# Performance work log

Measured on AMD Instinct MI355X. Metric: run time of the kernel, lower is better.

## Reference

```python
import jax, jax.numpy as jnp
import numpy as np

DIM = 128
NUM_HEADS = 8
HEAD_DIM = DIM // NUM_HEADS
N_NODES = 50000
N_EDGES = 800000


def setup_inputs() -> dict:
    key = jax.random.key(0)
    ks = jax.random.split(key, 10)
    scale = 1.0 / np.sqrt(DIM)
    x = jax.random.normal(ks[0], (N_NODES, DIM), dtype=jnp.float32)
    edge_index = jax.random.randint(ks[1], (2, N_EDGES), 0, N_NODES, dtype=jnp.int64)
    Wq = jax.random.normal(ks[2], (DIM, DIM), dtype=jnp.float32) * scale
    bq = jnp.zeros((DIM,), dtype=jnp.float32)
    Wk = jax.random.normal(ks[3], (DIM, DIM), dtype=jnp.float32) * scale
    bk = jnp.zeros((DIM,), dtype=jnp.float32)
    Wv = jax.random.normal(ks[4], (DIM, DIM), dtype=jnp.float32) * scale
    bv = jnp.zeros((DIM,), dtype=jnp.float32)
    Wo = jax.random.normal(ks[5], (DIM, DIM), dtype=jnp.float32) * scale
    bo = jnp.zeros((DIM,), dtype=jnp.float32)
    return {"x": x, "edge_index": edge_index, "Wq": Wq, "bq": bq,
            "Wk": Wk, "bk": bk, "Wv": Wv, "bv": bv, "Wo": Wo, "bo": bo}


def reference(x, edge_index, Wq, bq, Wk, bk, Wv, bv, Wo, bo):
    n = x.shape[0]
    tgt = edge_index[0]  # softmax group / scatter destination
    src = edge_index[1]  # gather source
    # projections: torch nn.Linear -> x @ W.T + b
    q = (x @ Wq.T + bq).reshape(n, NUM_HEADS, HEAD_DIM)
    k = (x @ Wk.T + bk).reshape(n, NUM_HEADS, HEAD_DIM)
    v = (x @ Wv.T + bv).reshape(n, NUM_HEADS, HEAD_DIM)
    # edge-wise attention scores: [E, H]
    scores = jnp.einsum('ehd,ehd->eh', q[src], k[tgt]) / np.sqrt(HEAD_DIM).astype(np.float32)
    # segment softmax over edges grouped by target node
    m = jax.ops.segment_max(scores, tgt, num_segments=n)          # [N, H]
    m = jax.lax.stop_gradient(m)
    p = jnp.exp(scores - m[tgt])                                   # [E, H]
    s = jax.ops.segment_sum(p, tgt, num_segments=n)               # [N, H]
    probs = p / s[tgt]
    # weighted scatter-add of source values
    weighted = v[src] * probs[..., None]                           # [E, H, D]
    agg = jax.ops.segment_sum(weighted, tgt, num_segments=n)      # [N, H, D]
    out = agg.reshape(n, DIM) @ Wo.T + bo
    # dropout is identity in eval mode
    return out
```

## Files before the change

kernel.cpp:

```cpp
#include <hip/hip_runtime.h>
#include <hip/hip_bf16.h>
#include <math.h>

#define NN 50000
#define NE 800000
#define DIM 128
#define NH 8
#define HD 16
#define NTILE 3125
#define TPB 782
#define LROW 136
#define QVROW 256
#define SCAN_B 196

typedef short v8s __attribute__((ext_vector_type(8)));
typedef float v4f __attribute__((ext_vector_type(4)));

__device__ __forceinline__ unsigned pack2(float a, float b) {
    __hip_bfloat162 h = __float22bfloat162_rn(make_float2(a, b));
    return *reinterpret_cast<unsigned*>(&h);
}
__device__ __forceinline__ float blo(unsigned w) { return __uint_as_float(w << 16); }
__device__ __forceinline__ float bhi(unsigned w) { return __uint_as_float(w & 0xffff0000u); }

__device__ __forceinline__ void stage_w_lds(
    const float* __restrict__ Wg, unsigned short* __restrict__ Wl, int tid)
{
#pragma unroll
    for (int it = 0; it < 16; ++it) {
        int chunk = it * 256 + tid;
        int row = chunk >> 5, c4 = chunk & 31;
        float4 f = ((const float4*)Wg)[chunk];
        uint2 o = { pack2(f.x, f.y), pack2(f.z, f.w) };
        *(uint2*)(Wl + row * LROW + c4 * 4) = o;
    }
}

__global__ __launch_bounds__(256) void qkv_mfma_kernel(
    const float* __restrict__ x,
    const float* __restrict__ Wq, const float* __restrict__ Wk, const float* __restrict__ Wv,
    const float* __restrict__ bq, const float* __restrict__ bk, const float* __restrict__ bv,
    unsigned short* __restrict__ qvb, unsigned short* __restrict__ kb,
    const int* __restrict__ tgt, int* __restrict__ cnt)
{
    __shared__ unsigned short Wl[DIM * LROW];
    const int mat = blockIdx.x / TPB;
    const int tg  = blockIdx.x % TPB;
    const int tid = threadIdx.x;
    const int lane = tid & 63;
    const int warp = tid >> 6;
    const int m = lane & 15;
    const int quad = lane >> 4;

    const int gsize = 3 * TPB * 256;
    for (int e = blockIdx.x * 256 + tid; e < NE; e += gsize)
        atomicAdd(cnt + tgt[e], 1);

    const float* Wg = (mat == 0) ? Wq : (mat == 1) ? Wk : Wv;
    stage_w_lds(Wg, Wl, tid);
    __syncthreads();

    const int rt = tg * 4 + warp;
    if (rt >= NTILE) return;
    const int r0 = rt * 16;
    const int node = r0 + m;

    const float* bias_p = (mat == 0) ? bq : (mat == 1) ? bk : bv;

    v8s a[4];
#pragma unroll
    for (int kt = 0; kt < 4; ++kt) {
        const float4* xr = (const float4*)(x + (size_t)node * DIM + kt * 32 + quad * 8);
        float4 f0 = xr[0], f1 = xr[1];
        uint4 u = { pack2(f0.x, f0.y), pack2(f0.z, f0.w),
                    pack2(f1.x, f1.y), pack2(f1.z, f1.w) };
        a[kt] = *(v8s*)&u;
    }

#pragma unroll
    for (int nt = 0; nt < 8; ++nt) {
        v4f c = {0.f, 0.f, 0.f, 0.f};
#pragma unroll
        for (int kt = 0; kt < 4; ++kt) {
            v8s wf = *(const v8s*)(Wl + (nt * 16 + m) * LROW + kt * 32 + quad * 8);
            c = __builtin_amdgcn_mfma_f32_16x16x32_bf16(wf, a[kt], c, 0, 0, 0);
        }
        const int cbase = nt * 16 + quad * 4;
        float4 b4 = *(const float4*)(bias_p + cbase);
        float o0 = c[0] + b4.x, o1 = c[1] + b4.y;
        float o2 = c[2] + b4.z, o3 = c[3] + b4.w;
        if (mat == 1) {
            uint2 pk = { pack2(o0, o1), pack2(o2, o3) };
            *(uint2*)(kb + (size_t)node * DIM + cbase) = pk;
        } else {
            int p0 = 2 * cbase + ((mat == 2) ? 2 : 0);
            *(unsigned*)(qvb + (size_t)node * QVROW + p0)     = pack2(o0, o1);
            *(unsigned*)(qvb + (size_t)node * QVROW + p0 + 4) = pack2(o2, o3);
        }
    }
}

__global__ __launch_bounds__(256) void scan1_kernel(
    const int* __restrict__ cnt, int* __restrict__ off, int* __restrict__ bsum)
{
    __shared__ int ws4[4];
    const int tid = threadIdx.x, lane = tid & 63, wid = tid >> 6;
    int i = blockIdx.x * 256 + tid;
    int v0 = (i < NN) ? cnt[i] : 0;
    int incl = v0;
#pragma unroll
    for (int d = 1; d < 64; d <<= 1) {
        int t = __shfl_up(incl, d);
        if (lane >= d) incl += t;
    }
    if (lane == 63) ws4[wid] = incl;
    __syncthreads();
    int wexcl = 0;
#pragma unroll
    for (int t = 0; t < 3; ++t) if (t < wid) wexcl += ws4[t];
    if (i < NN) off[i] = wexcl + incl - v0;
    if (tid == 255) bsum[blockIdx.x] = wexcl + incl;
}

__global__ __launch_bounds__(256) void scan23_kernel(
    const int* __restrict__ bsum, int* __restrict__ off, int* __restrict__ cursor)
{
    __shared__ int ws4[4];
    __shared__ int base_s, total_s;
    const int tid = threadIdx.x, lane = tid & 63, wid = tid >> 6;
    int v0 = (tid < SCAN_B) ? bsum[tid] : 0;
    int incl = v0;
#pragma unroll
    for (int d = 1; d < 64; d <<= 1) {
        int t = __shfl_up(incl, d);
        if (lane >= d) incl += t;
    }
    if (lane == 63) ws4[wid] = incl;
    __syncthreads();
    int wexcl = 0;
#pragma unroll
    for (int t = 0; t < 3; ++t) if (t < wid) wexcl += ws4[t];
    int excl = wexcl + incl - v0;
    if (tid == blockIdx.x) base_s = excl;
    if (tid == SCAN_B - 1) total_s = excl + v0;
    __syncthreads();
    int i = blockIdx.x * 256 + tid;
    if (i < NN) {
        int t = off[i] + base_s;
        off[i] = t;
        cursor[i] = t;
    }
    if (blockIdx.x == SCAN_B - 1 && tid == 0) off[NN] = total_s;
}

__global__ __launch_bounds__(256) void fill_kernel(
    const int* __restrict__ tgt, const int* __restrict__ src,
    int* __restrict__ cursor, int* __restrict__ edge_src)
{
    int e = blockIdx.x * 256 + threadIdx.x;
    if (e >= NE) return;
    int t = tgt[e];
    int pos = atomicAdd(cursor + t, 1);
    edge_src[pos] = src[e];
}

__global__ __launch_bounds__(256) void attn_kernel(
    const int* __restrict__ off, const int* __restrict__ edge_src,
    const unsigned short* __restrict__ qvb, const unsigned short* __restrict__ kb,
    unsigned short* __restrict__ aggb)
{
    __shared__ float red[2][64][3];
    const int tid = threadIdx.x;
    const int nib = tid >> 7;
    const int w   = (tid >> 6) & 1;
    const int lane = tid & 63;
    const int node = blockIdx.x * 2 + nib;

    const int base = off[node];
    const int deg  = off[node + 1] - base;

    unsigned kw = *(const unsigned*)(kb + (size_t)node * DIM + 2 * lane);
    const float klo = blo(kw), khi = bhi(kw);

    const int j = lane & 7;
    const int gb = lane & 56;

    float ax = 0.f, ay = 0.f, ss = 0.f;
    const int nw = (deg + 1 - w) >> 1;
    for (int c0 = 0; c0 < nw; c0 += 64) {
        int idx = c0 + lane;
        int srcv = edge_src[base + min(2 * idx + w, deg - 1)];
        int nchunk = min(nw - c0, 64);
        for (int b = 0; b < nchunk; b += 8) {
            int nb = min(nchunk - b, 8);
            uint2 qv[8];
#pragma unroll
            for (int i = 0; i < 8; ++i) {
                int si = __shfl(srcv, b + min(i, nb - 1));
                qv[i] = *(const uint2*)(qvb + (size_t)si * QVROW + 4 * lane);
            }
            float part[8];
#pragma unroll
            for (int i = 0; i < 8; ++i)
                part[i] = blo(qv[i].x) * klo + bhi(qv[i].x) * khi;
            float r1[4];
#pragma unroll
            for (int t = 0; t < 4; ++t) {
                float keep = (j & 1) ? part[2 * t + 1] : part[2 * t];
                float send = (j & 1) ? part[2 * t]     : part[2 * t + 1];
                r1[t] = keep + __shfl_xor(send, 1);
            }
            float r2[2];
#pragma unroll
            for (int u = 0; u < 2; ++u) {
                float keep = (j & 2) ? r1[2 * u + 1] : r1[2 * u];
                float send = (j & 2) ? r1[2 * u]     : r1[2 * u + 1];
                r2[u] = keep + __shfl_xor(send, 2);
            }
            float keep = (j & 4) ? r2[1] : r2[0];
            float send = (j & 4) ? r2[0] : r2[1];
            float tot = keep + __shfl_xor(send, 4);
            float p = __expf(tot * 0.25f);
#pragma unroll
            for (int i = 0; i < 8; ++i) {
                if (i < nb) {
                    float pi = __shfl(p, gb + i);
                    unsigned vv = qv[i].y;
                    ax += pi * blo(vv);
                    ay += pi * bhi(vv);
                    ss += pi;
                }
            }
        }
    }
    if (w == 1) {
        red[nib][lane][0] = ax; red[nib][lane][1] = ay; red[nib][lane][2] = ss;
    }
    __syncthreads();
    if (w == 0) {
        ax += red[nib][lane][0]; ay += red[nib][lane][1]; ss += red[nib][lane][2];
        unsigned* ap = (unsigned*)(aggb + (size_t)node * DIM + 2 * lane);
        if (deg == 0) {
            *ap = 0u;
        } else {
            float inv = 1.f / ss;
            *ap = pack2(ax * inv, ay * inv);
        }
    }
}

__global__ __launch_bounds__(256) void outproj_mfma_kernel(
    const unsigned short* __restrict__ aggb, const float* __restrict__ Wo,
    const float* __restrict__ bo, float* __restrict__ out)
{
    __shared__ unsigned short Wl[DIM * LROW];
    const int tid = threadIdx.x;
    const int lane = tid & 63;
    const int warp = tid >> 6;
    const int m = lane & 15;
    const int quad = lane >> 4;

    stage_w_lds(Wo, Wl, tid);
    __syncthreads();

    const int rt = blockIdx.x * 4 + warp;
    if (rt >= NTILE) return;
    const int r0 = rt * 16;
    const int node = r0 + m;

    v8s a[4];
#pragma unroll
    for (int kt = 0; kt < 4; ++kt)
        a[kt] = *(const v8s*)(aggb + (size_t)node * DIM + kt * 32 + quad * 8);

#pragma unroll
    for (int nt = 0; nt < 8; ++nt) {
        v4f c = {0.f, 0.f, 0.f, 0.f};
#pragma unroll
        for (int kt = 0; kt < 4; ++kt) {
            v8s wf = *(const v8s*)(Wl + (nt * 16 + m) * LROW + kt * 32 + quad * 8);
            c = __builtin_amdgcn_mfma_f32_16x16x32_bf16(wf, a[kt], c, 0, 0, 0);
        }
        const int cbase = nt * 16 + quad * 4;
        float4 b4 = *(const float4*)(bo + cbase);
        float4 o = { c[0] + b4.x, c[1] + b4.y, c[2] + b4.z, c[3] + b4.w };
        *(float4*)(out + (size_t)node * DIM + cbase) = o;
    }
}

extern "C" void kernel_launch(void* const* d_in, const int* in_sizes, int n_in,
                              void* d_out, int out_size, void* d_ws, size_t ws_size,
                              hipStream_t stream) {
    const float* x  = (const float*)d_in[0];
    const int*   ei = (const int*)d_in[1];
    const float* Wq = (const float*)d_in[2];
    const float* bq = (const float*)d_in[3];
    const float* Wk = (const float*)d_in[4];
    const float* bk = (const float*)d_in[5];
    const float* Wv = (const float*)d_in[6];
    const float* bv = (const float*)d_in[7];
    const float* Wo = (const float*)d_in[8];
    const float* bo = (const float*)d_in[9];

    const int* tgt = ei;
    const int* src = ei + NE;

    char* ws = (char*)d_ws;
    const size_t SZ_QV = (size_t)NN * QVROW * 2;
    const size_t SZ_BF = (size_t)NN * DIM * 2;

    unsigned short* qvb  = (unsigned short*)(ws);
    unsigned short* kb   = (unsigned short*)(ws + SZ_QV);
    unsigned short* aggb = (unsigned short*)(ws + SZ_QV + SZ_BF);

    char* wi = ws + SZ_QV + 2 * SZ_BF;
    int* cnt      = (int*)(wi);
    int* off      = (int*)(wi + (size_t)NN * 4);
    int* cursor   = (int*)(wi + (size_t)(2 * NN + 1) * 4);
    int* edge_src = (int*)(wi + (size_t)(3 * NN + 1) * 4);
    int* bsum     = (int*)(wi + (size_t)(3 * NN + 1) * 4 + (size_t)NE * 4);

    const int edge_blocks = (NE + 255) / 256;

    hipMemsetAsync(cnt, 0, (size_t)NN * 4, stream);
    qkv_mfma_kernel<<<3 * TPB, 256, 0, stream>>>(
        x, Wq, Wk, Wv, bq, bk, bv, qvb, kb, tgt, cnt);
    scan1_kernel<<<SCAN_B, 256, 0, stream>>>(cnt, off, bsum);
    scan23_kernel<<<SCAN_B, 256, 0, stream>>>(bsum, off, cursor);
    fill_kernel<<<edge_blocks, 256, 0, stream>>>(tgt, src, cursor, edge_src);
    attn_kernel<<<(NN + 1) / 2, 256, 0, stream>>>(off, edge_src, qvb, kb, aggb);
    outproj_mfma_kernel<<<TPB, 256, 0, stream>>>(aggb, Wo, bo, (float*)d_out);
}
```

Before: 267.3 us.

## Compute Q, V, K projections in one block reusing x fragments across weights

```diff
diff --git a/kernel.cpp b/kernel.cpp
--- a/kernel.cpp
+++ b/kernel.cpp
@@ -27,12 +27,14 @@
     const float* __restrict__ Wg, unsigned short* __restrict__ Wl, int tid)
 {
 #pragma unroll
-    for (int it = 0; it < 16; ++it) {
+    for (int it = 0; it < 8; ++it) {
         int chunk = it * 256 + tid;
-        int row = chunk >> 5, c4 = chunk & 31;
-        float4 f = ((const float4*)Wg)[chunk];
-        uint2 o = { pack2(f.x, f.y), pack2(f.z, f.w) };
-        *(uint2*)(Wl + row * LROW + c4 * 4) = o;
+        int row = chunk >> 4, c8 = chunk & 15;
+        float4 f0 = ((const float4*)Wg)[2 * chunk];
+        float4 f1 = ((const float4*)Wg)[2 * chunk + 1];
+        uint4 o = { pack2(f0.x, f0.y), pack2(f0.z, f0.w),
+                    pack2(f1.x, f1.y), pack2(f1.z, f1.w) };
+        *(uint4*)(Wl + row * LROW + c8 * 8) = o;
     }
 }
 
@@ -44,58 +46,89 @@
     const int* __restrict__ tgt, int* __restrict__ cnt)
 {
     __shared__ unsigned short Wl[DIM * LROW];
-    const int mat = blockIdx.x / TPB;
-    const int tg  = blockIdx.x % TPB;
     const int tid = threadIdx.x;
     const int lane = tid & 63;
     const int warp = tid >> 6;
     const int m = lane & 15;
     const int quad = lane >> 4;
 
-    const int gsize = 3 * TPB * 256;
+    const int gsize = TPB * 256;
     for (int e = blockIdx.x * 256 + tid; e < NE; e += gsize)
         atomicAdd(cnt + tgt[e], 1);
 
-    const float* Wg = (mat == 0) ? Wq : (mat == 1) ? Wk : Wv;
-    stage_w_lds(Wg, Wl, tid);
-    __syncthreads();
-
-    const int rt = tg * 4 + warp;
-    if (rt >= NTILE) return;
-    const int r0 = rt * 16;
-    const int node = r0 + m;
-
-    const float* bias_p = (mat == 0) ? bq : (mat == 1) ? bk : bv;
+    const int rt = blockIdx.x * 4 + warp;
+    const bool active = (rt < NTILE);
+    const int node = (active ? rt : 0) * 16 + m;
 
     v8s a[4];
-#pragma unroll
-    for (int kt = 0; kt < 4; ++kt) {
-        const float4* xr = (const float4*)(x + (size_t)node * DIM + kt * 32 + quad * 8);
-        float4 f0 = xr[0], f1 = xr[1];
-        uint4 u = { pack2(f0.x, f0.y), pack2(f0.z, f0.w),
-                    pack2(f1.x, f1.y), pack2(f1.z, f1.w) };
-        a[kt] = *(v8s*)&u;
-    }
-
-#pragma unroll
-    for (int nt = 0; nt < 8; ++nt) {
-        v4f c = {0.f, 0.f, 0.f, 0.f};
+    if (active) {
 #pragma unroll
         for (int kt = 0; kt < 4; ++kt) {
-            v8s wf = *(const v8s*)(Wl + (nt * 16 + m) * LROW + kt * 32 + quad * 8);
-            c = __builtin_amdgcn_mfma_f32_16x16x32_bf16(wf, a[kt], c, 0, 0, 0);
-        }
-        const int cbase = nt * 16 + quad * 4;
-        float4 b4 = *(const float4*)(bias_p + cbase);
-        float o0 = c[0] + b4.x, o1 = c[1] + b4.y;
-        float o2 = c[2] + b4.z, o3 = c[3] + b4.w;
-        if (mat == 1) {
-            uint2 pk = { pack2(o0, o1), pack2(o2, o3) };
+            const float4* xr = (const float4*)(x + (size_t)node * DIM + kt * 32 + quad * 8);
+            float4 f0 = xr[0], f1 = xr[1];
+            uint4 u = { pack2(f0.x, f0.y), pack2(f0.z, f0.w),
+                        pack2(f1.x, f1.y), pack2(f1.z, f1.w) };
+            a[kt] = *(v8s*)&u;
+        }
+    }
+
+    stage_w_lds(Wq, Wl, tid);
+    __syncthreads();
+    uint2 uq[8];
+    if (active) {
+#pragma unroll
+        for (int nt = 0; nt < 8; ++nt) {
+            v4f c = {0.f, 0.f, 0.f, 0.f};
+#pragma unroll
+            for (int kt = 0; kt < 4; ++kt) {
+                v8s wf = *(const v8s*)(Wl + (nt * 16 + m) * LROW + kt * 32 + quad * 8);
+                c = __builtin_amdgcn_mfma_f32_16x16x32_bf16(wf, a[kt], c, 0, 0, 0);
+            }
+            int cbase = nt * 16 + quad * 4;
+            float4 b4 = *(const float4*)(bq + cbase);
+            uq[nt].x = pack2(c[0] + b4.x, c[1] + b4.y);
+            uq[nt].y = pack2(c[2] + b4.z, c[3] + b4.w);
+        }
+    }
+    __syncthreads();
+
+    stage_w_lds(Wv, Wl, tid);
+    __syncthreads();
+    if (active) {
+#pragma unroll
+        for (int nt = 0; nt < 8; ++nt) {
+            v4f c = {0.f, 0.f, 0.f, 0.f};
+#pragma unroll
+            for (int kt = 0; kt < 4; ++kt) {
+                v8s wf = *(const v8s*)(Wl + (nt * 16 + m) * LROW + kt * 32 + quad * 8);
+                c = __builtin_amdgcn_mfma_f32_16x16x32_bf16(wf, a[kt], c, 0, 0, 0);
+            }
+            int cbase = nt * 16 + quad * 4;
+            float4 b4 = *(const float4*)(bv + cbase);
+            unsigned v01 = pack2(c[0] + b4.x, c[1] + b4.y);
+            unsigned v23 = pack2(c[2] + b4.z, c[3] + b4.w);
+            uint4 st = { uq[nt].x, v01, uq[nt].y, v23 };
+            *(uint4*)(qvb + (size_t)node * QVROW + 2 * cbase) = st;
+        }
+    }
+    __syncthreads();
+
+    stage_w_lds(Wk, Wl, tid);
+    __syncthreads();
+    if (active) {
+#pragma unroll
+        for (int nt = 0; nt < 8; ++nt) {
+            v4f c = {0.f, 0.f, 0.f, 0.f};
+#pragma unroll
+            for (int kt = 0; kt < 4; ++kt) {
+                v8s wf = *(const v8s*)(Wl + (nt * 16 + m) * LROW + kt * 32 + quad * 8);
+                c = __builtin_amdgcn_mfma_f32_16x16x32_bf16(wf, a[kt], c, 0, 0, 0);
+            }
+            int cbase = nt * 16 + quad * 4;
+            float4 b4 = *(const float4*)(bk + cbase);
+            uint2 pk = { pack2(c[0] + b4.x, c[1] + b4.y),
+                         pack2(c[2] + b4.z, c[3] + b4.w) };
             *(uint2*)(kb + (size_t)node * DIM + cbase) = pk;
-        } else {
-            int p0 = 2 * cbase + ((mat == 2) ? 2 : 0);
-            *(unsigned*)(qvb + (size_t)node * QVROW + p0)     = pack2(o0, o1);
-            *(unsigned*)(qvb + (size_t)node * QVROW + p0 + 4) = pack2(o2, o3);
         }
     }
 }
@@ -261,17 +294,19 @@
     const int quad = lane >> 4;
 
     stage_w_lds(Wo, Wl, tid);
-    __syncthreads();
 
     const int rt = blockIdx.x * 4 + warp;
-    if (rt >= NTILE) return;
-    const int r0 = rt * 16;
-    const int node = r0 + m;
+    const bool active = (rt < NTILE);
+    const int node = (active ? rt : 0) * 16 + m;
 
     v8s a[4];
-#pragma unroll
-    for (int kt = 0; kt < 4; ++kt)
-        a[kt] = *(const v8s*)(aggb + (size_t)node * DIM + kt * 32 + quad * 8);
+    if (active) {
+#pragma unroll
+        for (int kt = 0; kt < 4; ++kt)
+            a[kt] = *(const v8s*)(aggb + (size_t)node * DIM + kt * 32 + quad * 8);
+    }
+    __syncthreads();
+    if (!active) return;
 
 #pragma unroll
     for (int nt = 0; nt < 8; ++nt) {
@@ -323,7 +358,7 @@
     const int edge_blocks = (NE + 255) / 256;
 
     hipMemsetAsync(cnt, 0, (size_t)NN * 4, stream);
-    qkv_mfma_kernel<<<3 * TPB, 256, 0, stream>>>(
+    qkv_mfma_kernel<<<TPB, 256, 0, stream>>>(
         x, Wq, Wk, Wv, bq, bk, bv, qvb, kb, tgt, cnt);
     scan1_kernel<<<SCAN_B, 256, 0, stream>>>(cnt, off, bsum);
     scan23_kernel<<<SCAN_B, 256, 0, stream>>>(bsum, off, cursor);
```

New measurement: 258.8 us. 1.03x faster.
